# Optimization experiments

Measured on AMD Instinct MI355X. Metric: run time of the kernel, lower is better.

## Reference

```python
import jax, jax.numpy as jnp
import numpy as np

B, A, C, H, W = 2, 4, 3, 32, 32
N = H * W * A  # 4096 proposals
EPS = 1e-6


def setup_inputs() -> dict:
    key = jax.random.key(0)
    k1, k2, k3, k4 = jax.random.split(key, 4)
    scores = jax.random.normal(k1, (B, A * C, H, W), jnp.float32)
    bbox_preds = jax.random.normal(k2, (B, A * 7, H, W), jnp.float32)
    pp_params = jax.random.normal(k3, (B, C * 3, H, W), jnp.float32)
    # decoded LiDAR boxes (x, y, z, dx, dy, dz, yaw) with positive sizes
    u = jax.random.uniform(k4, (B, N, 7), jnp.float32)
    scale = jnp.array([80.0, 80.0, 4.0, 4.0, 4.0, 3.0, 6.28], jnp.float32)
    shift = jnp.array([-40.0, -40.0, -2.0, 0.5, 0.5, 0.5, -3.14], jnp.float32)
    decoded = u * scale + shift
    return {"scores": scores, "bbox_preds": bbox_preds,
            "pp_params": pp_params, "decoded": decoded}


def _nearest_bev(dec):
    # dec: [B, N, 7] -> axis-aligned nearest BEV boxes [B, N, 4] (x1,y1,x2,y2)
    bev = dec[..., jnp.array([0, 1, 3, 4, 6])]  # x, y, dx, dy, yaw
    rot = bev[..., 4]
    period = jnp.pi
    # limit_period(rot, offset=0.5, period=pi)
    normed = jnp.abs(rot - jnp.floor(rot / period + 0.5) * period)
    cond = (normed > jnp.pi / 4)[..., None]
    xywh = jnp.where(cond, bev[..., jnp.array([0, 1, 3, 2])], bev[..., :4])
    ctr, dims = xywh[..., :2], xywh[..., 2:]
    return jnp.concatenate([ctr - dims / 2, ctr + dims / 2], axis=-1)


def _pairwise_iou(boxes):
    # boxes: [B, N, 4] -> iou [B, N, N]
    lt = jnp.maximum(boxes[:, :, None, :2], boxes[:, None, :, :2])
    rb = jnp.minimum(boxes[:, :, None, 2:], boxes[:, None, :, 2:])
    wh = jnp.clip(rb - lt, 0.0)
    inter = wh[..., 0] * wh[..., 1]
    area = (boxes[..., 2] - boxes[..., 0]) * (boxes[..., 3] - boxes[..., 1])
    union = area[:, :, None] + area[:, None, :] - inter
    return inter / jnp.maximum(union, EPS)


def _forward_scores(scores, pp_params, decoded):
    # flatten scores: [B, A*C, H, W] -> [B, N, C]
    sc = scores.reshape(B, A, C, H, W).transpose(0, 3, 4, 1, 2).reshape(B, N, C)
    # flatten pp: [B, C*3, H, W] -> [B, H, W, C, 3] -> expand over A -> [B, N, C, 3]
    pp = pp_params.reshape(B, C, 3, H, W).transpose(0, 3, 4, 1, 2)
    pp = jnp.broadcast_to(pp[:, :, :, None], (B, H, W, A, C, 3)).reshape(B, N, C, 3)

    iou = _pairwise_iou(_nearest_bev(decoded[..., :7]))  # [B, N, N]
    sm_sc = jax.nn.softmax(sc, axis=1)  # softmax over proposal dim per class

    per_class = []
    for c in range(C):  # C is small and fixed
        p0 = pp[:, :, c, 0]
        p1 = pp[:, :, c, 1]
        weight = jax.nn.softmax(iou + p0[:, :, None] * p1[:, None, :], axis=2)
        per_class.append(jnp.einsum('bij,bj->bi', weight, sm_sc[:, :, c]))
    new_sc = jnp.stack(per_class, axis=-1)  # [B, N, C]

    # back to level layout: [B, N, C] -> [B, A*C, H, W]
    return new_sc.reshape(B, H, W, A, C).transpose(0, 3, 4, 1, 2).reshape(B, A * C, H, W)


def reference(scores, bbox_preds, pp_params, decoded):
    out_scores = _forward_scores(scores, pp_params, decoded)
    # original returns (out_scores_list, bbox_preds, dir_cls, pp_params); dir_cls=None
    return out_scores, bbox_preds, pp_params
```

## Files before the change

kernel.cpp:

```cpp
#include <hip/hip_runtime.h>
#include <math.h>

#define B_   2
#define C_   3
#define HW_  1024
#define N_   4096
#define AC_  12
#define JSPLIT 16
#define JTILE  256
#define ROWBLK 128
#define PI_F 3.14159265358979323846f
#define L2E     1.4426950408889634f
#define INV_L2E 0.6931471805599453f

#define OUT0_ELEMS 24576
#define OUT1_ELEMS 57344
#define OUT2_ELEMS 18432

#define WS_JBOX  0
#define WS_JAUX  32768
#define WS_JP1   65536
#define WS_JP0   98304
#define WS_PART  131072
#define WS_STATS 917504

#if __has_builtin(__builtin_amdgcn_exp2f)
#define EXP2F(x) __builtin_amdgcn_exp2f(x)
#else
#define EXP2F(x) __expf((x) * INV_L2E)
#endif

#define PREP_JBLKS 16
#define PREP_CPBLKS 80
#define CP_F4_BBOX 14336
#define CP_F4_TOT  18944

__device__ __forceinline__ float4 make_box(const float* __restrict__ d) {
    float x = d[0], y = d[1], d3 = d[3], d4 = d[4], rot = d[6];
    float kq = floorf(rot / PI_F + 0.5f);
    float normed = fabsf(rot - kq * PI_F);
    bool swap_wh = normed > (0.25f * PI_F);
    float w = swap_wh ? d4 : d3;
    float h = swap_wh ? d3 : d4;
    return make_float4(x - 0.5f * w, y - 0.5f * h, x + 0.5f * w, y + 0.5f * h);
}

__global__ __launch_bounds__(256) void k_prep(
    const float* __restrict__ scores, const float* __restrict__ pp,
    const float* __restrict__ dec, const float* __restrict__ bbox,
    float* __restrict__ ws, float* __restrict__ out)
{
    const int blk = blockIdx.x;
    const int t = threadIdx.x;

    if (blk >= PREP_JBLKS) {
        const float4* src1 = (const float4*)bbox;
        const float4* src2 = (const float4*)pp;
        float4* dst1 = (float4*)(out + OUT0_ELEMS);
        float4* dst2 = (float4*)(out + OUT0_ELEMS + OUT1_ELEMS);
        for (int u = (blk - PREP_JBLKS) * 256 + t; u < CP_F4_TOT;
             u += PREP_CPBLKS * 256) {
            if (u < CP_F4_BBOX) dst1[u] = src1[u];
            else                dst2[u - CP_F4_BBOX] = src2[u - CP_F4_BBOX];
        }
        return;
    }

    const int b = blk >> 3, seg = blk & 7;
    const float* decb = dec + b * N_ * 7;
    float4* jbox = (float4*)(ws + WS_JBOX) + b * N_;
    float4* jaux = (float4*)(ws + WS_JAUX) + b * N_;
    float4* jp1  = (float4*)(ws + WS_JP1)  + b * N_;
    float4* jp0  = (float4*)(ws + WS_JP0)  + b * N_;

    __shared__ float red[4][3];
    float ls0 = 0.f, ls1 = 0.f, ls2 = 0.f;
    const int n0 = seg * 512;
    for (int n = n0 + t; n < n0 + 512; n += 256) {
        const int hw = n >> 2, a = n & 3;
        float4 box = make_box(decb + n * 7);
        float area = (box.z - box.x) * (box.w - box.y);
        float e0 = __expf(scores[(b * AC_ + a * C_ + 0) * HW_ + hw]);
        float e1 = __expf(scores[(b * AC_ + a * C_ + 1) * HW_ + hw]);
        float e2 = __expf(scores[(b * AC_ + a * C_ + 2) * HW_ + hw]);
        ls0 += e0; ls1 += e1; ls2 += e2;
        jbox[n] = box;
        jaux[n] = make_float4(area * INV_L2E, e0, e1, e2);
        jp1[n]  = make_float4(pp[(b * 9 + 1) * HW_ + hw],
                              pp[(b * 9 + 4) * HW_ + hw],
                              pp[(b * 9 + 7) * HW_ + hw], 0.f);
        jp0[n]  = make_float4(pp[(b * 9 + 0) * HW_ + hw] * L2E,
                              pp[(b * 9 + 3) * HW_ + hw] * L2E,
                              pp[(b * 9 + 6) * HW_ + hw] * L2E, 0.f);
    }
#pragma unroll
    for (int off = 1; off < 64; off <<= 1) {
        ls0 += __shfl_xor(ls0, off);
        ls1 += __shfl_xor(ls1, off);
        ls2 += __shfl_xor(ls2, off);
    }
    if ((t & 63) == 0) { red[t >> 6][0] = ls0; red[t >> 6][1] = ls1; red[t >> 6][2] = ls2; }
    __syncthreads();
    if (t < 3)
        ws[WS_STATS + (b * C_ + t) * 8 + seg] =
            red[0][t] + red[1][t] + red[2][t] + red[3][t];
}

__global__ __launch_bounds__(256) void k_main(float* __restrict__ ws)
{
    const int b = blockIdx.y;
    const int jb = blockIdx.x & 15;
    const int rowblk = blockIdx.x >> 4;
    const int t = threadIdx.x;
    const int q = t >> 6;
    const int r = t & 63;

    const float4* jbox = (const float4*)(ws + WS_JBOX) + b * N_;
    const float4* jaux = (const float4*)(ws + WS_JAUX) + b * N_;
    const float4* jp1  = (const float4*)(ws + WS_JP1)  + b * N_;
    const float4* jp0  = (const float4*)(ws + WS_JP0)  + b * N_;

    __shared__ float4 s_box[JTILE];
    __shared__ float4 s_aux[JTILE];
    __shared__ float4 s_p1[JTILE];
    __shared__ float2 s_m[C_][ROWBLK][4];

    const int jbase = jb * JTILE;
    s_box[t] = jbox[jbase + t];
    s_aux[t] = jaux[jbase + t];
    s_p1[t]  = jp1[jbase + t];

    const int i0 = rowblk * ROWBLK + r, i1 = i0 + 64;
    const float4 bx0 = jbox[i0], bx1 = jbox[i1];
    const float  ar0 = jaux[i0].x, ar1 = jaux[i1].x;
    const float4 p0v0 = jp0[i0], p0v1 = jp0[i1];

    __syncthreads();

    float n00 = 0.f, d00 = 0.f, n01 = 0.f, d01 = 0.f, n02 = 0.f, d02 = 0.f;
    float n10 = 0.f, d10 = 0.f, n11 = 0.f, d11 = 0.f, n12 = 0.f, d12 = 0.f;

#pragma unroll 4
    for (int jj = q; jj < JTILE; jj += 4) {
        const float4 bj = s_box[jj];
        const float4 ax = s_aux[jj];
        const float4 pj = s_p1[jj];
        {
            float x1 = fmaxf(bx0.x, bj.x), y1 = fmaxf(bx0.y, bj.y);
            float x2 = fminf(bx0.z, bj.z), y2 = fminf(bx0.w, bj.w);
            float w = fmaxf(x2 - x1, 0.f), h = fmaxf(y2 - y1, 0.f);
            float inter = w * h;
            float uni = fmaf(inter, -INV_L2E, ar0 + ax.x);
            float iou = inter * __builtin_amdgcn_rcpf(uni);
            float e0 = EXP2F(fmaf(p0v0.x, pj.x, iou));
            float e1 = EXP2F(fmaf(p0v0.y, pj.y, iou));
            float e2 = EXP2F(fmaf(p0v0.z, pj.z, iou));
            n00 = fmaf(e0, ax.y, n00); d00 += e0;
            n01 = fmaf(e1, ax.z, n01); d01 += e1;
            n02 = fmaf(e2, ax.w, n02); d02 += e2;
        }
        {
            float x1 = fmaxf(bx1.x, bj.x), y1 = fmaxf(bx1.y, bj.y);
            float x2 = fminf(bx1.z, bj.z), y2 = fminf(bx1.w, bj.w);
            float w = fmaxf(x2 - x1, 0.f), h = fmaxf(y2 - y1, 0.f);
            float inter = w * h;
            float uni = fmaf(inter, -INV_L2E, ar1 + ax.x);
            float iou = inter * __builtin_amdgcn_rcpf(uni);
            float e0 = EXP2F(fmaf(p0v1.x, pj.x, iou));
            float e1 = EXP2F(fmaf(p0v1.y, pj.y, iou));
            float e2 = EXP2F(fmaf(p0v1.z, pj.z, iou));
            n10 = fmaf(e0, ax.y, n10); d10 += e0;
            n11 = fmaf(e1, ax.z, n11); d11 += e1;
            n12 = fmaf(e2, ax.w, n12); d12 += e2;
        }
    }

    s_m[0][r][q] = make_float2(n00, d00);
    s_m[1][r][q] = make_float2(n01, d01);
    s_m[2][r][q] = make_float2(n02, d02);
    s_m[0][r + 64][q] = make_float2(n10, d10);
    s_m[1][r + 64][q] = make_float2(n11, d11);
    s_m[2][r + 64][q] = make_float2(n12, d12);
    __syncthreads();

    float2* part = (float2*)(ws + WS_PART);
    for (int u = t; u < C_ * ROWBLK; u += 256) {
        const int c = u >> 7, row = u & 127;
        float2 a0 = s_m[c][row][0], a1 = s_m[c][row][1];
        float2 a2 = s_m[c][row][2], a3 = s_m[c][row][3];
        part[((b * JSPLIT + jb) * C_ + c) * N_ + rowblk * ROWBLK + row] =
            make_float2(a0.x + a1.x + a2.x + a3.x, a0.y + a1.y + a2.y + a3.y);
    }
}

__global__ __launch_bounds__(256) void k_reduce(
    const float* __restrict__ ws, float* __restrict__ out)
{
    const int tid = blockIdx.x * 256 + threadIdx.x;
    const int bc = tid >> 12;
    const int i  = tid & 4095;
    const int b = bc / C_, c = bc % C_;
    const float2* part = (const float2*)(ws + WS_PART);
    float num = 0.f, den = 0.f;
#pragma unroll
    for (int jb = 0; jb < JSPLIT; ++jb) {
        float2 v = part[((b * JSPLIT + jb) * C_ + c) * N_ + i];
        num += v.x; den += v.y;
    }
    float S = 0.f;
#pragma unroll
    for (int s = 0; s < 8; ++s) S += ws[WS_STATS + bc * 8 + s];
    out[(b * AC_ + (i & 3) * 3 + c) * HW_ + (i >> 2)] = num / (den * S);
}

extern "C" void kernel_launch(void* const* d_in, const int* in_sizes, int n_in,
                              void* d_out, int out_size, void* d_ws, size_t ws_size,
                              hipStream_t stream) {
    const float* scores = (const float*)d_in[0];
    const float* bbox   = (const float*)d_in[1];
    const float* pp     = (const float*)d_in[2];
    const float* dec    = (const float*)d_in[3];
    float* out = (float*)d_out;
    float* ws  = (float*)d_ws;

    k_prep<<<PREP_JBLKS + PREP_CPBLKS, 256, 0, stream>>>(scores, pp, dec, bbox, ws, out);
    k_main<<<dim3(32 * JSPLIT, B_), 256, 0, stream>>>(ws);
    k_reduce<<<OUT0_ELEMS / 256, 256, 0, stream>>>(ws, out);
}
```

Baseline: 93.77 us.

## Fuse prep, main and reduce into one kernel with in-block column recompute

Replaces the three-kernel pipeline (prep to workspace, split-J main writing partials, reduce) with a single kernel. Each block owns 32 rows and sweeps all 4096 columns in 512-wide tiles, recomputing boxes, exps and pp terms per tile from the raw inputs, with register prefetch of the next tile. The per-class score sum is accumulated in the same sweep. This removes two launches and the workspace round-trips, but every block now redoes the column preprocessing and only 256 compute blocks are launched.

```diff
diff --git a/kernel.cpp b/kernel.cpp
--- a/kernel.cpp
+++ b/kernel.cpp
@@ -6,10 +6,8 @@
 #define HW_  1024
 #define N_   4096
 #define AC_  12
-#define JSPLIT 16
-#define JTILE  256
-#define ROWBLK 128
-#define PI_F 3.14159265358979323846f
+
+#define PI_F    3.14159265358979323846f
 #define L2E     1.4426950408889634f
 #define INV_L2E 0.6931471805599453f
 
@@ -17,23 +15,19 @@
 #define OUT1_ELEMS 57344
 #define OUT2_ELEMS 18432
 
-#define WS_JBOX  0
-#define WS_JAUX  32768
-#define WS_JP1   65536
-#define WS_JP0   98304
-#define WS_PART  131072
-#define WS_STATS 917504
+#define ROWBLK   32
+#define JTILE    512
+#define NTILE    8
+#define MAINBLKS 256
+#define CPBLKS   32
+#define CP_F4_BBOX 14336
+#define CP_F4_TOT  18944
 
 #if __has_builtin(__builtin_amdgcn_exp2f)
 #define EXP2F(x) __builtin_amdgcn_exp2f(x)
 #else
 #define EXP2F(x) __expf((x) * INV_L2E)
 #endif
-
-#define PREP_JBLKS 16
-#define PREP_CPBLKS 80
-#define CP_F4_BBOX 14336
-#define CP_F4_TOT  18944
 
 __device__ __forceinline__ float4 make_box(const float* __restrict__ d) {
     float x = d[0], y = d[1], d3 = d[3], d4 = d[4], rot = d[6];
@@ -45,185 +39,179 @@
     return make_float4(x - 0.5f * w, y - 0.5f * h, x + 0.5f * w, y + 0.5f * h);
 }
 
-__global__ __launch_bounds__(256) void k_prep(
+__global__ __launch_bounds__(512) void k_fused(
     const float* __restrict__ scores, const float* __restrict__ pp,
     const float* __restrict__ dec, const float* __restrict__ bbox,
-    float* __restrict__ ws, float* __restrict__ out)
+    float* __restrict__ out)
 {
     const int blk = blockIdx.x;
     const int t = threadIdx.x;
 
-    if (blk >= PREP_JBLKS) {
+    if (blk >= MAINBLKS) {
         const float4* src1 = (const float4*)bbox;
         const float4* src2 = (const float4*)pp;
         float4* dst1 = (float4*)(out + OUT0_ELEMS);
         float4* dst2 = (float4*)(out + OUT0_ELEMS + OUT1_ELEMS);
-        for (int u = (blk - PREP_JBLKS) * 256 + t; u < CP_F4_TOT;
-             u += PREP_CPBLKS * 256) {
+        for (int u = (blk - MAINBLKS) * 512 + t; u < CP_F4_TOT;
+             u += CPBLKS * 512) {
             if (u < CP_F4_BBOX) dst1[u] = src1[u];
             else                dst2[u - CP_F4_BBOX] = src2[u - CP_F4_BBOX];
         }
         return;
     }
 
-    const int b = blk >> 3, seg = blk & 7;
-    const float* decb = dec + b * N_ * 7;
-    float4* jbox = (float4*)(ws + WS_JBOX) + b * N_;
-    float4* jaux = (float4*)(ws + WS_JAUX) + b * N_;
-    float4* jp1  = (float4*)(ws + WS_JP1)  + b * N_;
-    float4* jp0  = (float4*)(ws + WS_JP0)  + b * N_;
-
-    __shared__ float red[4][3];
-    float ls0 = 0.f, ls1 = 0.f, ls2 = 0.f;
-    const int n0 = seg * 512;
-    for (int n = n0 + t; n < n0 + 512; n += 256) {
-        const int hw = n >> 2, a = n & 3;
-        float4 box = make_box(decb + n * 7);
-        float area = (box.z - box.x) * (box.w - box.y);
-        float e0 = __expf(scores[(b * AC_ + a * C_ + 0) * HW_ + hw]);
-        float e1 = __expf(scores[(b * AC_ + a * C_ + 1) * HW_ + hw]);
-        float e2 = __expf(scores[(b * AC_ + a * C_ + 2) * HW_ + hw]);
-        ls0 += e0; ls1 += e1; ls2 += e2;
-        jbox[n] = box;
-        jaux[n] = make_float4(area * INV_L2E, e0, e1, e2);
-        jp1[n]  = make_float4(pp[(b * 9 + 1) * HW_ + hw],
-                              pp[(b * 9 + 4) * HW_ + hw],
-                              pp[(b * 9 + 7) * HW_ + hw], 0.f);
-        jp0[n]  = make_float4(pp[(b * 9 + 0) * HW_ + hw] * L2E,
-                              pp[(b * 9 + 3) * HW_ + hw] * L2E,
-                              pp[(b * 9 + 6) * HW_ + hw] * L2E, 0.f);
-    }
-#pragma unroll
-    for (int off = 1; off < 64; off <<= 1) {
-        ls0 += __shfl_xor(ls0, off);
-        ls1 += __shfl_xor(ls1, off);
-        ls2 += __shfl_xor(ls2, off);
-    }
-    if ((t & 63) == 0) { red[t >> 6][0] = ls0; red[t >> 6][1] = ls1; red[t >> 6][2] = ls2; }
-    __syncthreads();
-    if (t < 3)
-        ws[WS_STATS + (b * C_ + t) * 8 + seg] =
-            red[0][t] + red[1][t] + red[2][t] + red[3][t];
-}
-
-__global__ __launch_bounds__(256) void k_main(float* __restrict__ ws)
-{
-    const int b = blockIdx.y;
-    const int jb = blockIdx.x & 15;
-    const int rowblk = blockIdx.x >> 4;
-    const int t = threadIdx.x;
-    const int q = t >> 6;
-    const int r = t & 63;
-
-    const float4* jbox = (const float4*)(ws + WS_JBOX) + b * N_;
-    const float4* jaux = (const float4*)(ws + WS_JAUX) + b * N_;
-    const float4* jp1  = (const float4*)(ws + WS_JP1)  + b * N_;
-    const float4* jp0  = (const float4*)(ws + WS_JP0)  + b * N_;
+    const int b = blk >> 7;
+    const int rowblk = blk & 127;
+    const int r = t & 15;
+    const int q = t >> 4;
+
+    const float* __restrict__ decb = dec + b * (N_ * 7);
+    const float* __restrict__ scb  = scores + b * (AC_ * HW_);
+    const float* __restrict__ ppb  = pp + b * (9 * HW_);
 
     __shared__ float4 s_box[JTILE];
     __shared__ float4 s_aux[JTILE];
     __shared__ float4 s_p1[JTILE];
-    __shared__ float2 s_m[C_][ROWBLK][4];
-
-    const int jbase = jb * JTILE;
-    s_box[t] = jbox[jbase + t];
-    s_aux[t] = jaux[jbase + t];
-    s_p1[t]  = jp1[jbase + t];
-
-    const int i0 = rowblk * ROWBLK + r, i1 = i0 + 64;
-    const float4 bx0 = jbox[i0], bx1 = jbox[i1];
-    const float  ar0 = jaux[i0].x, ar1 = jaux[i1].x;
-    const float4 p0v0 = jp0[i0], p0v1 = jp0[i1];
-
-    __syncthreads();
+    __shared__ float2 s_red[8][16][C_][2];
+    __shared__ float  s_Sp[8][C_];
+
+    const int i0 = rowblk * ROWBLK + r, i1 = i0 + 16;
+    const float4 bx0 = make_box(decb + i0 * 7);
+    const float4 bx1 = make_box(decb + i1 * 7);
+    const float ar0 = (bx0.z - bx0.x) * (bx0.w - bx0.y) * INV_L2E;
+    const float ar1 = (bx1.z - bx1.x) * (bx1.w - bx1.y) * INV_L2E;
+    const int hw0 = i0 >> 2, hw1 = i1 >> 2;
+    const float p00x = ppb[0 * HW_ + hw0] * L2E;
+    const float p00y = ppb[3 * HW_ + hw0] * L2E;
+    const float p00z = ppb[6 * HW_ + hw0] * L2E;
+    const float p01x = ppb[0 * HW_ + hw1] * L2E;
+    const float p01y = ppb[3 * HW_ + hw1] * L2E;
+    const float p01z = ppb[6 * HW_ + hw1] * L2E;
 
     float n00 = 0.f, d00 = 0.f, n01 = 0.f, d01 = 0.f, n02 = 0.f, d02 = 0.f;
     float n10 = 0.f, d10 = 0.f, n11 = 0.f, d11 = 0.f, n12 = 0.f, d12 = 0.f;
-
+    float sS0 = 0.f, sS1 = 0.f, sS2 = 0.f;
+
+    float ld0, ld1, ld3, ld4, ld6, ls0, ls1, ls2, lp1a, lp1b, lp1c;
+    {
+        const float* dj = decb + t * 7;
+        ld0 = dj[0]; ld1 = dj[1]; ld3 = dj[3]; ld4 = dj[4]; ld6 = dj[6];
+        const int hw = t >> 2, a = t & 3;
+        ls0 = scb[(a * C_ + 0) * HW_ + hw];
+        ls1 = scb[(a * C_ + 1) * HW_ + hw];
+        ls2 = scb[(a * C_ + 2) * HW_ + hw];
+        lp1a = ppb[1 * HW_ + hw]; lp1b = ppb[4 * HW_ + hw]; lp1c = ppb[7 * HW_ + hw];
+    }
+
+    for (int tile = 0; tile < NTILE; ++tile) {
+        if (tile) __syncthreads();
+        {
+            float kq = floorf(ld6 / PI_F + 0.5f);
+            float normed = fabsf(ld6 - kq * PI_F);
+            bool sw = normed > (0.25f * PI_F);
+            float w = sw ? ld4 : ld3, h = sw ? ld3 : ld4;
+            float4 box = make_float4(ld0 - 0.5f * w, ld1 - 0.5f * h,
+                                     ld0 + 0.5f * w, ld1 + 0.5f * h);
+            float area = (box.z - box.x) * (box.w - box.y);
+            float e0 = __expf(ls0), e1 = __expf(ls1), e2 = __expf(ls2);
+            sS0 += e0; sS1 += e1; sS2 += e2;
+            s_box[t] = box;
+            s_aux[t] = make_float4(area * INV_L2E, e0, e1, e2);
+            s_p1[t]  = make_float4(lp1a, lp1b, lp1c, 0.f);
+        }
+        __syncthreads();
+        if (tile + 1 < NTILE) {
+            const int j = (tile + 1) * JTILE + t;
+            const float* dj = decb + j * 7;
+            ld0 = dj[0]; ld1 = dj[1]; ld3 = dj[3]; ld4 = dj[4]; ld6 = dj[6];
+            const int hw = j >> 2, a = j & 3;
+            ls0 = scb[(a * C_ + 0) * HW_ + hw];
+            ls1 = scb[(a * C_ + 1) * HW_ + hw];
+            ls2 = scb[(a * C_ + 2) * HW_ + hw];
+            lp1a = ppb[1 * HW_ + hw]; lp1b = ppb[4 * HW_ + hw]; lp1c = ppb[7 * HW_ + hw];
+        }
 #pragma unroll 4
-    for (int jj = q; jj < JTILE; jj += 4) {
-        const float4 bj = s_box[jj];
-        const float4 ax = s_aux[jj];
-        const float4 pj = s_p1[jj];
-        {
-            float x1 = fmaxf(bx0.x, bj.x), y1 = fmaxf(bx0.y, bj.y);
-            float x2 = fminf(bx0.z, bj.z), y2 = fminf(bx0.w, bj.w);
-            float w = fmaxf(x2 - x1, 0.f), h = fmaxf(y2 - y1, 0.f);
-            float inter = w * h;
-            float uni = fmaf(inter, -INV_L2E, ar0 + ax.x);
-            float iou = inter * __builtin_amdgcn_rcpf(uni);
-            float e0 = EXP2F(fmaf(p0v0.x, pj.x, iou));
-            float e1 = EXP2F(fmaf(p0v0.y, pj.y, iou));
-            float e2 = EXP2F(fmaf(p0v0.z, pj.z, iou));
-            n00 = fmaf(e0, ax.y, n00); d00 += e0;
-            n01 = fmaf(e1, ax.z, n01); d01 += e1;
-            n02 = fmaf(e2, ax.w, n02); d02 += e2;
-        }
-        {
-            float x1 = fmaxf(bx1.x, bj.x), y1 = fmaxf(bx1.y, bj.y);
-            float x2 = fminf(bx1.z, bj.z), y2 = fminf(bx1.w, bj.w);
-            float w = fmaxf(x2 - x1, 0.f), h = fmaxf(y2 - y1, 0.f);
-            float inter = w * h;
-            float uni = fmaf(inter, -INV_L2E, ar1 + ax.x);
-            float iou = inter * __builtin_amdgcn_rcpf(uni);
-            float e0 = EXP2F(fmaf(p0v1.x, pj.x, iou));
-            float e1 = EXP2F(fmaf(p0v1.y, pj.y, iou));
-            float e2 = EXP2F(fmaf(p0v1.z, pj.z, iou));
-            n10 = fmaf(e0, ax.y, n10); d10 += e0;
-            n11 = fmaf(e1, ax.z, n11); d11 += e1;
-            n12 = fmaf(e2, ax.w, n12); d12 += e2;
-        }
-    }
-
-    s_m[0][r][q] = make_float2(n00, d00);
-    s_m[1][r][q] = make_float2(n01, d01);
-    s_m[2][r][q] = make_float2(n02, d02);
-    s_m[0][r + 64][q] = make_float2(n10, d10);
-    s_m[1][r + 64][q] = make_float2(n11, d11);
-    s_m[2][r + 64][q] = make_float2(n12, d12);
+        for (int m = 0; m < 16; ++m) {
+            const int jj = q + (m << 5);
+            const float4 bj = s_box[jj];
+            const float4 ax = s_aux[jj];
+            const float4 pj = s_p1[jj];
+            {
+                float x1 = fmaxf(bx0.x, bj.x), y1 = fmaxf(bx0.y, bj.y);
+                float x2 = fminf(bx0.z, bj.z), y2 = fminf(bx0.w, bj.w);
+                float w = fmaxf(x2 - x1, 0.f), h = fmaxf(y2 - y1, 0.f);
+                float inter = w * h;
+                float uni = fmaf(inter, -INV_L2E, ar0 + ax.x);
+                float iou = inter * __builtin_amdgcn_rcpf(uni);
+                float e0 = EXP2F(fmaf(p00x, pj.x, iou));
+                float e1 = EXP2F(fmaf(p00y, pj.y, iou));
+                float e2 = EXP2F(fmaf(p00z, pj.z, iou));
+                n00 = fmaf(e0, ax.y, n00); d00 += e0;
+                n01 = fmaf(e1, ax.z, n01); d01 += e1;
+                n02 = fmaf(e2, ax.w, n02); d02 += e2;
+            }
+            {
+                float x1 = fmaxf(bx1.x, bj.x), y1 = fmaxf(bx1.y, bj.y);
+                float x2 = fminf(bx1.z, bj.z), y2 = fminf(bx1.w, bj.w);
+                float w = fmaxf(x2 - x1, 0.f), h = fmaxf(y2 - y1, 0.f);
+                float inter = w * h;
+                float uni = fmaf(inter, -INV_L2E, ar1 + ax.x);
+                float iou = inter * __builtin_amdgcn_rcpf(uni);
+                float e0 = EXP2F(fmaf(p01x, pj.x, iou));
+                float e1 = EXP2F(fmaf(p01y, pj.y, iou));
+                float e2 = EXP2F(fmaf(p01z, pj.z, iou));
+                n10 = fmaf(e0, ax.y, n10); d10 += e0;
+                n11 = fmaf(e1, ax.z, n11); d11 += e1;
+                n12 = fmaf(e2, ax.w, n12); d12 += e2;
+            }
+        }
+    }
+
+#define RED4(v) { v += __shfl_xor(v, 16); v += __shfl_xor(v, 32); }
+    RED4(n00) RED4(d00) RED4(n01) RED4(d01) RED4(n02) RED4(d02)
+    RED4(n10) RED4(d10) RED4(n11) RED4(d11) RED4(n12) RED4(d12)
+#undef RED4
+    const int wv = t >> 6, lane = t & 63;
+    if (lane < 16) {
+        s_red[wv][lane][0][0] = make_float2(n00, d00);
+        s_red[wv][lane][1][0] = make_float2(n01, d01);
+        s_red[wv][lane][2][0] = make_float2(n02, d02);
+        s_red[wv][lane][0][1] = make_float2(n10, d10);
+        s_red[wv][lane][1][1] = make_float2(n11, d11);
+        s_red[wv][lane][2][1] = make_float2(n12, d12);
+    }
+#pragma unroll
+    for (int off = 1; off < 64; off <<= 1) {
+        sS0 += __shfl_xor(sS0, off);
+        sS1 += __shfl_xor(sS1, off);
+        sS2 += __shfl_xor(sS2, off);
+    }
+    if (lane == 0) { s_Sp[wv][0] = sS0; s_Sp[wv][1] = sS1; s_Sp[wv][2] = sS2; }
     __syncthreads();
 
-    float2* part = (float2*)(ws + WS_PART);
-    for (int u = t; u < C_ * ROWBLK; u += 256) {
-        const int c = u >> 7, row = u & 127;
-        float2 a0 = s_m[c][row][0], a1 = s_m[c][row][1];
-        float2 a2 = s_m[c][row][2], a3 = s_m[c][row][3];
-        part[((b * JSPLIT + jb) * C_ + c) * N_ + rowblk * ROWBLK + row] =
-            make_float2(a0.x + a1.x + a2.x + a3.x, a0.y + a1.y + a2.y + a3.y);
-    }
-}
-
-__global__ __launch_bounds__(256) void k_reduce(
-    const float* __restrict__ ws, float* __restrict__ out)
-{
-    const int tid = blockIdx.x * 256 + threadIdx.x;
-    const int bc = tid >> 12;
-    const int i  = tid & 4095;
-    const int b = bc / C_, c = bc % C_;
-    const float2* part = (const float2*)(ws + WS_PART);
-    float num = 0.f, den = 0.f;
+    if (t < C_ * ROWBLK) {
+        const int c = t >> 5, row = t & 31;
+        const int rr = row & 15, half = row >> 4;
+        float num = 0.f, den = 0.f, S = 0.f;
 #pragma unroll
-    for (int jb = 0; jb < JSPLIT; ++jb) {
-        float2 v = part[((b * JSPLIT + jb) * C_ + c) * N_ + i];
-        num += v.x; den += v.y;
-    }
-    float S = 0.f;
-#pragma unroll
-    for (int s = 0; s < 8; ++s) S += ws[WS_STATS + bc * 8 + s];
-    out[(b * AC_ + (i & 3) * 3 + c) * HW_ + (i >> 2)] = num / (den * S);
+        for (int w = 0; w < 8; ++w) {
+            float2 v = s_red[w][rr][c][half];
+            num += v.x; den += v.y;
+            S += s_Sp[w][c];
+        }
+        const int n = rowblk * ROWBLK + half * 16 + rr;
+        out[(b * AC_ + (n & 3) * C_ + c) * HW_ + (n >> 2)] = num / (den * S);
+    }
 }
 
 extern "C" void kernel_launch(void* const* d_in, const int* in_sizes, int n_in,
                               void* d_out, int out_size, void* d_ws, size_t ws_size,
                               hipStream_t stream) {
+    (void)d_ws; (void)ws_size;
     const float* scores = (const float*)d_in[0];
     const float* bbox   = (const float*)d_in[1];
     const float* pp     = (const float*)d_in[2];
     const float* dec    = (const float*)d_in[3];
-    float* out = (float*)d_out;
-    float* ws  = (float*)d_ws;
-
-    k_prep<<<PREP_JBLKS + PREP_CPBLKS, 256, 0, stream>>>(scores, pp, dec, bbox, ws, out);
-    k_main<<<dim3(32 * JSPLIT, B_), 256, 0, stream>>>(ws);
-    k_reduce<<<OUT0_ELEMS / 256, 256, 0, stream>>>(ws, out);
+    k_fused<<<MAINBLKS + CPBLKS, 512, 0, stream>>>(
+        scores, pp, dec, bbox, (float*)d_out);
 }
```

New measurement: 92.58 us. Within noise of the previous version (-1.3%).
